# Optimization experiments

Hardware: AMD Instinct MI355X
Metric: run time of the kernel (lower is better)

The kernel has to match this reference:

```python
import jax, jax.numpy as jnp
import numpy as np

VOCAB = 32000
HIDDEN = 512


def setup_inputs() -> dict:
    key = jax.random.key(0)
    k1, k2, k3, k4 = jax.random.split(key, 4)
    B, L = 64, 2048  # batch of trees, leaves per (complete binary) tree
    leaf_ids = jax.random.randint(k1, (B, L), 0, VOCAB)
    emb = jax.random.normal(k2, (VOCAB, HIDDEN), dtype=jnp.float32)
    # nn.Linear(2H, H): weight [H, 2H], bias [H]
    lim = 1.0 / np.sqrt(2 * HIDDEN)
    W = jax.random.uniform(k3, (HIDDEN, 2 * HIDDEN), minval=-lim, maxval=lim, dtype=jnp.float32)
    b = jax.random.uniform(k4, (HIDDEN,), minval=-lim, maxval=lim, dtype=jnp.float32)
    return {"leaf_ids": leaf_ids, "emb": emb, "W": W, "b": b}


def reference(leaf_ids, emb, W, b):
    # Preterminal nodes: embed leaf token then activation (matches original order).
    h = jnp.tanh(emb[leaf_ids])  # [B, L, H]
    B, L, H = h.shape
    n_levels = int(np.log2(L))
    # Bottom-up: each internal node concatenates its two children -> linear -> tanh.
    # All same-depth nodes processed as one batched GEMM.
    for _ in range(n_levels):
        n = h.shape[1]
        pairs = h.reshape(B, n // 2, 2 * H)          # concat(left, right) along feature dim
        h = jnp.tanh(jnp.einsum('bnf,hf->bnh', pairs, W) + b)
    return h  # [B, 1, H] root hidden state per tree
```

## Files before the change

### kernel.cpp

```cpp
#include <hip/hip_runtime.h>
#include <stdint.h>

typedef __attribute__((ext_vector_type(8))) short short8;
typedef __attribute__((ext_vector_type(4))) float floatx4;

__device__ __forceinline__ unsigned short f2bf(float x) {
    unsigned int u = __builtin_bit_cast(unsigned int, x);
    unsigned int r = (u + 0x7FFFu + ((u >> 16) & 1u)) >> 16;
    return (unsigned short)r;
}
__device__ __forceinline__ float bf2f(unsigned short x) {
    unsigned int u = ((unsigned int)x) << 16;
    return __builtin_bit_cast(float, u);
}

__device__ __forceinline__ float fast_tanh(float x) {
    float xc = fminf(fmaxf(x, -10.0f), 10.0f);
    float e  = __expf(2.0f * xc);
    float d  = e + 1.0f;
    float r  = __builtin_amdgcn_rcpf(d);
    r = r * (2.0f - d * r);
    return (e - 1.0f) * r;
}

__global__ void wconv(const float4* __restrict__ W4, ushort4* __restrict__ Wb4) {
    int i = blockIdx.x * 256 + threadIdx.x;
    float4 v = W4[i];
    ushort4 o;
    o.x = f2bf(v.x); o.y = f2bf(v.y); o.z = f2bf(v.z); o.w = f2bf(v.w);
    Wb4[i] = o;
}

__global__ void tconv(const float4* __restrict__ emb4, ushort4* __restrict__ embT4) {
    int i = blockIdx.x * 256 + threadIdx.x;
    float4 v = emb4[i];
    ushort4 o;
    o.x = f2bf(fast_tanh(v.x)); o.y = f2bf(fast_tanh(v.y));
    o.z = f2bf(fast_tanh(v.z)); o.w = f2bf(fast_tanh(v.w));
    embT4[i] = o;
}

__global__ void lvl1_add(const int* __restrict__ ids, const ushort* __restrict__ PQ,
                         const float* __restrict__ bias, ushort* __restrict__ h1)
{
    int idx = blockIdx.x * 256 + threadIdx.x;
    int m = idx >> 6;
    int c = (idx & 63) << 3;
    const int il = ids[2 * m], ir = ids[2 * m + 1];
    const short8 p = *reinterpret_cast<const short8*>(PQ + (size_t)il * 512 + c);
    const short8 q = *reinterpret_cast<const short8*>(PQ + 16384000 + (size_t)ir * 512 + c);
    const float4 b0 = *reinterpret_cast<const float4*>(bias + c);
    const float4 b1 = *reinterpret_cast<const float4*>(bias + c + 4);
    short8 o;
    o[0] = (short)f2bf(fast_tanh(bf2f((unsigned short)p[0]) + bf2f((unsigned short)q[0]) + b0.x));
    o[1] = (short)f2bf(fast_tanh(bf2f((unsigned short)p[1]) + bf2f((unsigned short)q[1]) + b0.y));
    o[2] = (short)f2bf(fast_tanh(bf2f((unsigned short)p[2]) + bf2f((unsigned short)q[2]) + b0.z));
    o[3] = (short)f2bf(fast_tanh(bf2f((unsigned short)p[3]) + bf2f((unsigned short)q[3]) + b0.w));
    o[4] = (short)f2bf(fast_tanh(bf2f((unsigned short)p[4]) + bf2f((unsigned short)q[4]) + b1.x));
    o[5] = (short)f2bf(fast_tanh(bf2f((unsigned short)p[5]) + bf2f((unsigned short)q[5]) + b1.y));
    o[6] = (short)f2bf(fast_tanh(bf2f((unsigned short)p[6]) + bf2f((unsigned short)q[6]) + b1.z));
    o[7] = (short)f2bf(fast_tanh(bf2f((unsigned short)p[7]) + bf2f((unsigned short)q[7]) + b1.w));
    *reinterpret_cast<short8*>(h1 + (size_t)idx * 8) = o;
}

#define STG264(buf, k0)                                                         \
    do {                                                                        \
        _Pragma("unroll")                                                       \
        for (int p = 0; p < 4; ++p) {                                           \
            __builtin_amdgcn_global_load_lds(                                   \
                (const __attribute__((address_space(1))) void*)(Ap + (size_t)p * 64 * ASTR + (k0)), \
                (__attribute__((address_space(3))) void*)&sA[buf][p * 4096 + tid * 8], 16, 0, 0); \
            __builtin_amdgcn_global_load_lds(                                   \
                (const __attribute__((address_space(1))) void*)(Bp + (size_t)p * 64 * 1024 + (k0)), \
                (__attribute__((address_space(3))) void*)&sB[buf][p * 4096 + tid * 8], 16, 0, 0); \
        }                                                                       \
    } while (0)

#define CMP264(buf)                                                             \
    do {                                                                        \
        _Pragma("unroll")                                                       \
        for (int ks = 0; ks < 2; ++ks) {                                        \
            const int kq_ = ks * 4 + lh;                                        \
            const int sw_ = ((kq_ ^ (l15 & 7)) << 3);                           \
            short8 a_[8], b_[4];                                                \
            _Pragma("unroll")                                                   \
            for (int ni = 0; ni < 4; ++ni)                                      \
                b_[ni] = *reinterpret_cast<const short8*>(&sB[buf][(rB + ni * 16) * 64 + sw_]); \
            _Pragma("unroll")                                                   \
            for (int mi = 0; mi < 8; ++mi)                                      \
                a_[mi] = *reinterpret_cast<const short8*>(&sA[buf][(rA + mi * 16) * 64 + sw_]); \
            __builtin_amdgcn_s_setprio(1);                                      \
            _Pragma("unroll")                                                   \
            for (int mi = 0; mi < 8; ++mi)                                      \
                _Pragma("unroll")                                               \
                for (int ni = 0; ni < 4; ++ni)                                  \
                    acc[mi][ni] = __builtin_amdgcn_mfma_f32_16x16x32_bf16(      \
                        a_[mi], b_[ni], acc[mi][ni], 0, 0, 0);                  \
            __builtin_amdgcn_s_setprio(0);                                      \
        }                                                                       \
    } while (0)

template<int ASTR, int NT, int MODE>
__global__ __launch_bounds__(512)
void gemm256(const ushort* __restrict__ A, const ushort* __restrict__ Bt,
             const float* __restrict__ bias, ushort* __restrict__ outb)
{
    __shared__ alignas(16) ushort sA[2][16384];
    __shared__ alignas(16) ushort sB[2][16384];

    const int tid  = threadIdx.x;
    const int lane = tid & 63;
    const int w    = tid >> 6;
    const int wr   = w >> 2, wc = w & 3;
    const int l15  = lane & 15;
    const int lh   = lane >> 4;

    int mt, ntile, koff = 0;
    size_t obase = 0;
    if constexpr (MODE == 0) {
        const int nb  = gridDim.x;
        const int per = nb >> 3;
        const int lin = (blockIdx.x & 7) * per + (blockIdx.x >> 3);
        mt = lin >> 1; ntile = lin & 1;
    } else {
        int bid = blockIdx.x;
        const int table = (bid >= 250) ? 1 : 0;
        const int rem = bid - table * 250;
        mt = rem >> 1; ntile = rem & 1;
        koff  = table << 9;
        obase = (size_t)table * 16384000;
    }
    const int m0 = mt * 256, n0 = ntile * 256;

    const int r0 = tid >> 3;
    const int s0 = tid & 7;
    const int swz = ((s0 ^ (r0 & 7)) << 3);
    const ushort* Ap = A  + (size_t)(m0 + r0) * ASTR + swz;
    const ushort* Bp = Bt + (size_t)(n0 + r0) * 1024 + koff + swz;

    const int rA = wr * 128 + l15;
    const int rB = wc * 64  + l15;

    floatx4 acc[8][4] = {};

    STG264(0, 0);
    for (int t = 0; t + 2 < NT; t += 2) {
        asm volatile("s_barrier" ::: "memory");
        STG264(1, (t + 1) * 64);
        asm volatile("s_waitcnt vmcnt(8)" ::: "memory");
        CMP264(0);
        asm volatile("s_barrier" ::: "memory");
        STG264(0, (t + 2) * 64);
        asm volatile("s_waitcnt vmcnt(8)" ::: "memory");
        CMP264(1);
    }
    asm volatile("s_barrier" ::: "memory");
    STG264(1, (NT - 1) * 64);
    asm volatile("s_waitcnt vmcnt(8)" ::: "memory");
    CMP264(0);
    asm volatile("s_barrier" ::: "memory");
    asm volatile("s_waitcnt vmcnt(0)" ::: "memory");
    CMP264(1);

    const int mrow = lh * 4;
    #pragma unroll
    for (int mi = 0; mi < 8; ++mi) {
        #pragma unroll
        for (int ni = 0; ni < 4; ++ni) {
            const int n = n0 + wc * 64 + ni * 16 + l15;
            #pragma unroll
            for (int j = 0; j < 4; ++j) {
                const int m = m0 + wr * 128 + mi * 16 + mrow + j;
                if constexpr (MODE == 0) {
                    float v = fast_tanh(acc[mi][ni][j] + bias[n]);
                    outb[(size_t)m * 512 + n] = f2bf(v);
                } else {
                    outb[obase + (size_t)m * 512 + n] = f2bf(acc[mi][ni][j]);
                }
            }
        }
    }
}

#define STAGE_(buf, k0)                                                         \
    do {                                                                        \
        __builtin_amdgcn_global_load_lds(                                       \
            (const __attribute__((address_space(1))) void*)(Ap + (k0)),         \
            (__attribute__((address_space(3))) void*)&sA[buf][tid * 8], 16, 0, 0); \
        __builtin_amdgcn_global_load_lds(                                       \
            (const __attribute__((address_space(1))) void*)(Ap + 64 * 1024 + (k0)), \
            (__attribute__((address_space(3))) void*)&sA[buf][2048 + tid * 8], 16, 0, 0); \
        __builtin_amdgcn_global_load_lds(                                       \
            (const __attribute__((address_space(1))) void*)(Bp + (k0)),         \
            (__attribute__((address_space(3))) void*)&sB[buf][tid * 8], 16, 0, 0); \
        __builtin_amdgcn_global_load_lds(                                       \
            (const __attribute__((address_space(1))) void*)(Bp + 64 * 1024 + (k0)), \
            (__attribute__((address_space(3))) void*)&sB[buf][2048 + tid * 8], 16, 0, 0); \
    } while (0)

#define COMPUTE_(cur)                                                           \
    do {                                                                        \
        short8 a_[4], b_[4];                                                    \
        _Pragma("unroll")                                                       \
        for (int mi = 0; mi < 4; ++mi)                                          \
            a_[mi] = *reinterpret_cast<const short8*>(&sA[cur][(rA + mi * 16) * 32 + kksw]); \
        _Pragma("unroll")                                                       \
        for (int ni = 0; ni < 4; ++ni)                                          \
            b_[ni] = *reinterpret_cast<const short8*>(&sB[cur][(rB + ni * 16) * 32 + kksw]); \
        __builtin_amdgcn_s_setprio(1);                                          \
        _Pragma("unroll")                                                       \
        for (int mi = 0; mi < 4; ++mi)                                          \
            _Pragma("unroll")                                                   \
            for (int ni = 0; ni < 4; ++ni)                                      \
                acc[mi][ni] = __builtin_amdgcn_mfma_f32_16x16x32_bf16(          \
                    a_[mi], b_[ni], acc[mi][ni], 0, 0, 0);                      \
        __builtin_amdgcn_s_setprio(0);                                          \
    } while (0)

__global__ __launch_bounds__(256)
void level_gemm(const ushort* __restrict__ A, const ushort* __restrict__ Bt,
                const float* __restrict__ bias,
                ushort* __restrict__ outb, int M)
{
    const int nb  = gridDim.x;
    int bid = blockIdx.x;
    const int per = nb >> 3;
    const int lin = (bid & 7) * per + (bid >> 3);
    const int mt = lin >> 2, nt = lin & 3;
    const int m0 = mt * 128, n0 = nt * 128;

    __shared__ alignas(16) ushort sA[3][4096];
    __shared__ alignas(16) ushort sB[3][4096];

    const int tid  = threadIdx.x;
    const int lane = tid & 63;
    const int w    = tid >> 6;
    const int wr   = w >> 1, wc = w & 1;

    const int sr    = tid >> 2;
    const int swcol = (((tid & 3) ^ ((tid >> 3) & 3)) << 3);
    const ushort* Ap = A  + (size_t)(m0 + sr) * 1024 + swcol;
    const ushort* Bp = Bt + (size_t)(n0 + sr) * 1024 + swcol;

    const int rA   = wr * 64 + (lane & 15);
    const int rB   = wc * 64 + (lane & 15);
    const int kksw = (((lane >> 4) ^ ((lane >> 1) & 3)) << 3);

    floatx4 acc[4][4] = {};

    STAGE_(0, 0);
    STAGE_(1, 32);
    for (int t = 0; t < 30; t += 3) {
        asm volatile("s_barrier" ::: "memory");
        STAGE_(2, (t + 2) * 32);
        asm volatile("s_waitcnt vmcnt(4)" ::: "memory");
        COMPUTE_(0);
        asm volatile("s_barrier" ::: "memory");
        STAGE_(0, (t + 3) * 32);
        asm volatile("s_waitcnt vmcnt(4)" ::: "memory");
        COMPUTE_(1);
        asm volatile("s_barrier" ::: "memory");
        STAGE_(1, (t + 4) * 32);
        asm volatile("s_waitcnt vmcnt(4)" ::: "memory");
        COMPUTE_(2);
    }
    asm volatile("s_barrier" ::: "memory");
    asm volatile("s_waitcnt vmcnt(0)" ::: "memory");
    COMPUTE_(0);
    asm volatile("s_barrier" ::: "memory");
    asm volatile("s_waitcnt vmcnt(0)" ::: "memory");
    COMPUTE_(1);

    const int mrow = (lane >> 4) * 4;
    const int ncol = lane & 15;
    #pragma unroll
    for (int mi = 0; mi < 4; ++mi)
        #pragma unroll
        for (int ni = 0; ni < 4; ++ni) {
            const int n = n0 + wc * 64 + ni * 16 + ncol;
            const float bb = bias[n];
            #pragma unroll
            for (int j = 0; j < 4; ++j) {
                const int m = m0 + wr * 64 + mi * 16 + mrow + j;
                float v = fast_tanh(acc[mi][ni][j] + bb);
                outb[(size_t)m * 512 + n] = f2bf(v);
            }
        }
}

__global__ __launch_bounds__(256)
void small_gemm(const ushort* __restrict__ A, const ushort* __restrict__ Bt,
                const float* __restrict__ bias,
                ushort* __restrict__ outb, float* __restrict__ outf, int last)
{
    __shared__ alignas(16) ushort sA[3][4096];
    __shared__ alignas(16) ushort sB[3][4096];

    const int tid  = threadIdx.x;
    const int lane = tid & 63;
    const int w    = tid >> 6;
    const int l15  = lane & 15;
    const int lh   = lane >> 4;
    const int mt   = blockIdx.x >> 3, nt = blockIdx.x & 7;
    const int m0   = mt * 64, n0 = nt * 64;

    const int r0 = tid >> 3;
    const int s0 = tid & 7;
    const int swz = ((s0 ^ (r0 & 7)) << 3);
    const ushort* Ap = A  + (size_t)(m0 + r0) * 1024 + swz;
    const ushort* Bp = Bt + (size_t)(n0 + r0) * 1024 + swz;

#define STG6(buf, k0)                                                           \
    do {                                                                        \
        __builtin_amdgcn_global_load_lds(                                       \
            (const __attribute__((address_space(1))) void*)(Ap + (k0)),         \
            (__attribute__((address_space(3))) void*)&sA[buf][tid * 8], 16, 0, 0); \
        __builtin_amdgcn_global_load_lds(                                       \
            (const __attribute__((address_space(1))) void*)(Ap + 32 * 1024 + (k0)), \
            (__attribute__((address_space(3))) void*)&sA[buf][2048 + tid * 8], 16, 0, 0); \
        __builtin_amdgcn_global_load_lds(                                       \
            (const __attribute__((address_space(1))) void*)(Bp + (k0)),         \
            (__attribute__((address_space(3))) void*)&sB[buf][tid * 8], 16, 0, 0); \
        __builtin_amdgcn_global_load_lds(                                       \
            (const __attribute__((address_space(1))) void*)(Bp + 32 * 1024 + (k0)), \
            (__attribute__((address_space(3))) void*)&sB[buf][2048 + tid * 8], 16, 0, 0); \
    } while (0)

    const int rb = w * 16 + l15;
    floatx4 acc[4] = {};

#define CMP6(buf)                                                               \
    do {                                                                        \
        _Pragma("unroll")                                                       \
        for (int ks = 0; ks < 2; ++ks) {                                        \
            const int kq = ks * 4 + lh;                                         \
            const short8 b_ = *reinterpret_cast<const short8*>(                 \
                &sB[buf][rb * 64 + ((kq ^ (rb & 7)) << 3)]);                    \
            __builtin_amdgcn_s_setprio(1);                                      \
            _Pragma("unroll")                                                   \
            for (int mi = 0; mi < 4; ++mi) {                                    \
                const int ra = mi * 16 + l15;                                   \
                const short8 a_ = *reinterpret_cast<const short8*>(             \
                    &sA[buf][ra * 64 + ((kq ^ (l15 & 7)) << 3)]);               \
                acc[mi] = __builtin_amdgcn_mfma_f32_16x16x32_bf16(              \
                    a_, b_, acc[mi], 0, 0, 0);                                  \
            }                                                                   \
            __builtin_amdgcn_s_setprio(0);                                      \
        }                                                                       \
    } while (0)

    STG6(0, 0);
    STG6(1, 64);
    for (int t3 = 0; t3 < 12; t3 += 3) {
        asm volatile("s_barrier" ::: "memory");
        STG6(2, (t3 + 2) * 64);
        asm volatile("s_waitcnt vmcnt(4)" ::: "memory");
        CMP6(0);
        asm volatile("s_barrier" ::: "memory");
        STG6(0, (t3 + 3) * 64);
        asm volatile("s_waitcnt vmcnt(4)" ::: "memory");
        CMP6(1);
        asm volatile("s_barrier" ::: "memory");
        STG6(1, (t3 + 4) * 64);
        asm volatile("s_waitcnt vmcnt(4)" ::: "memory");
        CMP6(2);
    }
    asm volatile("s_barrier" ::: "memory");
    STG6(2, 14 * 64);
    asm volatile("s_waitcnt vmcnt(8)" ::: "memory");
    CMP6(0);
    asm volatile("s_barrier" ::: "memory");
    STG6(0, 15 * 64);
    asm volatile("s_waitcnt vmcnt(8)" ::: "memory");
    CMP6(1);
    asm volatile("s_barrier" ::: "memory");
    asm volatile("s_waitcnt vmcnt(4)" ::: "memory");
    CMP6(2);
    asm volatile("s_barrier" ::: "memory");
    asm volatile("s_waitcnt vmcnt(0)" ::: "memory");
    CMP6(0);
#undef CMP6
#undef STG6

    const int n  = n0 + w * 16 + l15;
    const float bb = bias[n];
    #pragma unroll
    for (int mi = 0; mi < 4; ++mi) {
        #pragma unroll
        for (int j = 0; j < 4; ++j) {
            const int m = m0 + mi * 16 + lh * 4 + j;
            float v = fast_tanh(acc[mi][j] + bb);
            if (last) outf[(size_t)m * 512 + n] = v;
            else      outb[(size_t)m * 512 + n] = f2bf(v);
        }
    }
}

extern "C" void kernel_launch(void* const* d_in, const int* in_sizes, int n_in,
                              void* d_out, int out_size, void* d_ws, size_t ws_size,
                              hipStream_t stream) {
    const int*   ids  = (const int*)d_in[0];
    const float* emb  = (const float*)d_in[1];
    const float* W    = (const float*)d_in[2];
    const float* bias = (const float*)d_in[3];
    float* out = (float*)d_out;

    unsigned short* Wb   = (unsigned short*)d_ws;
    unsigned short* embT = Wb + 524288;
    unsigned short* PQ   = embT + 16384000;
    unsigned short* hB   = PQ + 32768000;
    unsigned short* hA   = hB + 33554432;

    wconv<<<512, 256, 0, stream>>>((const float4*)W, (ushort4*)Wb);
    tconv<<<16000, 256, 0, stream>>>((const float4*)emb, (ushort4*)embT);

    gemm256<512, 8, 1><<<500, 512, 0, stream>>>(embT, Wb, bias, PQ);
    lvl1_add<<<16384, 256, 0, stream>>>(ids, PQ, bias, hB);

    gemm256<1024, 16, 0><<<256, 512, 0, stream>>>(hB, Wb, bias, hA);

    level_gemm<<<512, 256, 0, stream>>>(hA, Wb, bias, hB, 16384);
    level_gemm<<<256, 256, 0, stream>>>(hB, Wb, bias, hA, 8192);

    int M = 4096;
    for (int l = 5; l <= 11; ++l) {
        const unsigned short* in = (l & 1) ? hA : hB;
        unsigned short*       ob = (l & 1) ? hB : hA;
        small_gemm<<<(M / 64) * 8, 256, 0, stream>>>(in, Wb, bias, ob, out,
                                                     l == 11 ? 1 : 0);
        M >>= 1;
    }
}
```

Before: 260.7 us.

## Restructure gemm256 into 4-stage K=32 LDS pipeline with new swizzle

Replaces the double-buffered K=64 LDS staging in gemm256 with a four-buffer ring of K=32 tiles, keeping three tiles in flight ahead of compute. It changes the staging thread mapping, the XOR swizzle and the per-tile loop structure, and doubles NT at the call sites to match. The aim is to hide global-to-LDS latency better at the same LDS footprint, at the cost of twice as many barriers per K and smaller MFMA batches between syncs.

```diff
diff --git a/kernel.cpp b/kernel.cpp
--- a/kernel.cpp
+++ b/kernel.cpp
@@ -63,41 +63,47 @@
     *reinterpret_cast<short8*>(h1 + (size_t)idx * 8) = o;
 }
 
-#define STG264(buf, k0)                                                         \
-    do {                                                                        \
-        _Pragma("unroll")                                                       \
-        for (int p = 0; p < 4; ++p) {                                           \
-            __builtin_amdgcn_global_load_lds(                                   \
-                (const __attribute__((address_space(1))) void*)(Ap + (size_t)p * 64 * ASTR + (k0)), \
-                (__attribute__((address_space(3))) void*)&sA[buf][p * 4096 + tid * 8], 16, 0, 0); \
-            __builtin_amdgcn_global_load_lds(                                   \
-                (const __attribute__((address_space(1))) void*)(Bp + (size_t)p * 64 * 1024 + (k0)), \
-                (__attribute__((address_space(3))) void*)&sB[buf][p * 4096 + tid * 8], 16, 0, 0); \
-        }                                                                       \
-    } while (0)
-
-#define CMP264(buf)                                                             \
-    do {                                                                        \
-        _Pragma("unroll")                                                       \
-        for (int ks = 0; ks < 2; ++ks) {                                        \
-            const int kq_ = ks * 4 + lh;                                        \
-            const int sw_ = ((kq_ ^ (l15 & 7)) << 3);                           \
-            short8 a_[8], b_[4];                                                \
+#define STG4(buf, t)                                                            \
+    do {                                                                        \
+        __builtin_amdgcn_global_load_lds(                                       \
+            (const __attribute__((address_space(1))) void*)(Ap + (t) * 32),     \
+            (__attribute__((address_space(3))) void*)&sA[buf][tid * 8], 16, 0, 0); \
+        __builtin_amdgcn_global_load_lds(                                       \
+            (const __attribute__((address_space(1))) void*)(Ap + (size_t)128 * ASTR + (t) * 32), \
+            (__attribute__((address_space(3))) void*)&sA[buf][4096 + tid * 8], 16, 0, 0); \
+        __builtin_amdgcn_global_load_lds(                                       \
+            (const __attribute__((address_space(1))) void*)(Bp + (t) * 32),     \
+            (__attribute__((address_space(3))) void*)&sB[buf][tid * 8], 16, 0, 0); \
+        __builtin_amdgcn_global_load_lds(                                       \
+            (const __attribute__((address_space(1))) void*)(Bp + 128 * 1024 + (t) * 32), \
+            (__attribute__((address_space(3))) void*)&sB[buf][4096 + tid * 8], 16, 0, 0); \
+    } while (0)
+
+#define CMP4(buf)                                                               \
+    do {                                                                        \
+        short8 a_[8], b_[4];                                                    \
+        _Pragma("unroll")                                                       \
+        for (int mi = 0; mi < 8; ++mi)                                          \
+            a_[mi] = *reinterpret_cast<const short8*>(&sA[buf][(rA + mi * 16) * 32 + kksw]); \
+        _Pragma("unroll")                                                       \
+        for (int ni = 0; ni < 4; ++ni)                                          \
+            b_[ni] = *reinterpret_cast<const short8*>(&sB[buf][(rB + ni * 16) * 32 + kksw]); \
+        __builtin_amdgcn_s_setprio(1);                                          \
+        _Pragma("unroll")                                                       \
+        for (int mi = 0; mi < 8; ++mi)                                          \
             _Pragma("unroll")                                                   \
             for (int ni = 0; ni < 4; ++ni)                                      \
-                b_[ni] = *reinterpret_cast<const short8*>(&sB[buf][(rB + ni * 16) * 64 + sw_]); \
-            _Pragma("unroll")                                                   \
-            for (int mi = 0; mi < 8; ++mi)                                      \
-                a_[mi] = *reinterpret_cast<const short8*>(&sA[buf][(rA + mi * 16) * 64 + sw_]); \
-            __builtin_amdgcn_s_setprio(1);                                      \
-            _Pragma("unroll")                                                   \
-            for (int mi = 0; mi < 8; ++mi)                                      \
-                _Pragma("unroll")                                               \
-                for (int ni = 0; ni < 4; ++ni)                                  \
-                    acc[mi][ni] = __builtin_amdgcn_mfma_f32_16x16x32_bf16(      \
-                        a_[mi], b_[ni], acc[mi][ni], 0, 0, 0);                  \
-            __builtin_amdgcn_s_setprio(0);                                      \
-        }                                                                       \
+                acc[mi][ni] = __builtin_amdgcn_mfma_f32_16x16x32_bf16(          \
+                    a_[mi], b_[ni], acc[mi][ni], 0, 0, 0);                      \
+        __builtin_amdgcn_s_setprio(0);                                          \
+    } while (0)
+
+#define ITER4(sbuf, tile, cbuf)                                                 \
+    do {                                                                        \
+        asm volatile("s_barrier" ::: "memory");                                 \
+        STG4(sbuf, tile);                                                       \
+        asm volatile("s_waitcnt vmcnt(8)" ::: "memory");                        \
+        CMP4(cbuf);                                                             \
     } while (0)
 
 template<int ASTR, int NT, int MODE>
@@ -105,8 +111,8 @@
 void gemm256(const ushort* __restrict__ A, const ushort* __restrict__ Bt,
              const float* __restrict__ bias, ushort* __restrict__ outb)
 {
-    __shared__ alignas(16) ushort sA[2][16384];
-    __shared__ alignas(16) ushort sB[2][16384];
+    __shared__ alignas(16) ushort sA[4][8192];
+    __shared__ alignas(16) ushort sB[4][8192];
 
     const int tid  = threadIdx.x;
     const int lane = tid & 63;
@@ -132,35 +138,38 @@
     }
     const int m0 = mt * 256, n0 = ntile * 256;
 
-    const int r0 = tid >> 3;
-    const int s0 = tid & 7;
-    const int swz = ((s0 ^ (r0 & 7)) << 3);
-    const ushort* Ap = A  + (size_t)(m0 + r0) * ASTR + swz;
-    const ushort* Bp = Bt + (size_t)(n0 + r0) * 1024 + koff + swz;
-
-    const int rA = wr * 128 + l15;
-    const int rB = wc * 64  + l15;
+    const int sr    = tid >> 2;
+    const int swcol = (((tid & 3) ^ ((tid >> 3) & 3)) << 3);
+    const ushort* Ap = A  + (size_t)(m0 + sr) * ASTR + swcol;
+    const ushort* Bp = Bt + (size_t)(n0 + sr) * 1024 + koff + swcol;
+
+    const int rA   = wr * 128 + l15;
+    const int rB   = wc * 64  + l15;
+    const int kksw = ((lh ^ ((lane >> 1) & 3)) << 3);
 
     floatx4 acc[8][4] = {};
 
-    STG264(0, 0);
-    for (int t = 0; t + 2 < NT; t += 2) {
-        asm volatile("s_barrier" ::: "memory");
-        STG264(1, (t + 1) * 64);
-        asm volatile("s_waitcnt vmcnt(8)" ::: "memory");
-        CMP264(0);
-        asm volatile("s_barrier" ::: "memory");
-        STG264(0, (t + 2) * 64);
-        asm volatile("s_waitcnt vmcnt(8)" ::: "memory");
-        CMP264(1);
-    }
-    asm volatile("s_barrier" ::: "memory");
-    STG264(1, (NT - 1) * 64);
+    STG4(0, 0);
+    STG4(1, 1);
+    STG4(2, 2);
     asm volatile("s_waitcnt vmcnt(8)" ::: "memory");
-    CMP264(0);
+
+    for (int t = 0; t < NT - 4; t += 4) {
+        ITER4(3, t + 3, 0);
+        ITER4(0, t + 4, 1);
+        ITER4(1, t + 5, 2);
+        ITER4(2, t + 6, 3);
+    }
+    ITER4(3, NT - 1, 0);
+    asm volatile("s_barrier" ::: "memory");
+    asm volatile("s_waitcnt vmcnt(8)" ::: "memory");
+    CMP4(1);
+    asm volatile("s_barrier" ::: "memory");
+    asm volatile("s_waitcnt vmcnt(4)" ::: "memory");
+    CMP4(2);
     asm volatile("s_barrier" ::: "memory");
     asm volatile("s_waitcnt vmcnt(0)" ::: "memory");
-    CMP264(1);
+    CMP4(3);
 
     const int mrow = lh * 4;
     #pragma unroll
@@ -414,10 +423,10 @@
     wconv<<<512, 256, 0, stream>>>((const float4*)W, (ushort4*)Wb);
     tconv<<<16000, 256, 0, stream>>>((const float4*)emb, (ushort4*)embT);
 
-    gemm256<512, 8, 1><<<500, 512, 0, stream>>>(embT, Wb, bias, PQ);
+    gemm256<512, 16, 1><<<500, 512, 0, stream>>>(embT, Wb, bias, PQ);
     lvl1_add<<<16384, 256, 0, stream>>>(ids, PQ, bias, hB);
 
-    gemm256<1024, 16, 0><<<256, 512, 0, stream>>>(hB, Wb, bias, hA);
+    gemm256<1024, 32, 0><<<256, 512, 0, stream>>>(hB, Wb, bias, hA);
 
     level_gemm<<<512, 256, 0, stream>>>(hA, Wb, bias, hB, 16384);
     level_gemm<<<256, 256, 0, stream>>>(hB, Wb, bias, hA, 8192);
```

New measurement: 267.3 us. 1.03x slower.
